# Performance work log

Measured on AMD Instinct MI355X. Metric: run time of the kernel, lower is better.

## Reference

```python
import jax, jax.numpy as jnp
import numpy as np

N = 50000      # nodes
E = 800000     # edges (avg degree 16)
DIN = 128
DH = 128
DOUT = 40
ALPHA = 0.1
BETA = 1.0


def gcn_conv(x, src, dst, ew, W, b, n):
    """PyG GCNConv: add self-loops, symmetric deg^-1/2 normalization, gather-scatter."""
    idx = jnp.arange(n)
    s = jnp.concatenate([src, idx])
    d = jnp.concatenate([dst, idx])
    w = jnp.concatenate([ew, jnp.ones((n,), x.dtype)])
    deg = jax.ops.segment_sum(w, d, num_segments=n)            # [N]
    dinv = jnp.where(deg > 0, jax.lax.rsqrt(deg), 0.0)
    norm = dinv[s] * w * dinv[d]                               # [E+N]
    h = x @ W                                                  # [N, dout]
    msg = h[s] * norm[:, None]                                 # gather + scale
    out = jax.ops.segment_sum(msg, d, num_segments=n)          # scatter-add
    return out + b


def setup_inputs() -> dict:
    key = jax.random.key(0)
    ks = jax.random.split(key, 10)
    x = jax.random.normal(ks[0], (N, DIN), jnp.float32)
    edge_index = jax.random.randint(ks[1], (2, E), 0, N, dtype=jnp.int64)
    edge_weight = jax.random.uniform(ks[2], (E,), jnp.float32)
    W1 = jax.random.normal(ks[3], (DIN, DH), jnp.float32) / np.float32(np.sqrt(DIN))
    b1 = jnp.zeros((DH,), jnp.float32)
    W2 = jax.random.normal(ks[4], (DH, DH), jnp.float32) / np.float32(np.sqrt(DH))
    b2 = jnp.zeros((DH,), jnp.float32)
    W3 = jax.random.normal(ks[5], (DH, DOUT), jnp.float32) / np.float32(np.sqrt(DH))
    b3 = jnp.zeros((DOUT,), jnp.float32)
    return {"x": x, "edge_index": edge_index, "edge_weight": edge_weight,
            "W1": W1, "b1": b1, "W2": W2, "b2": b2, "W3": W3, "b3": b3}


def reference(x, edge_index, edge_weight, W1, b1, W2, b2, W3, b3):
    src, dst = edge_index[0], edge_index[1]
    ones_w = jnp.ones((E,), x.dtype)
    h1 = jax.nn.relu(gcn_conv(x, src, dst, ones_w, W1, b1, N))   # conv1 (edge_weight=None)
    hc = gcn_conv(h1, src, dst, edge_weight, W2, b2, N)          # crf_layer with edge_weight
    h = ALPHA * h1 + BETA * hc                                   # weighted residual combo
    # LearnableBernoulliDropout: identity in eval mode
    out = gcn_conv(h, src, dst, ones_w, W3, b3, N)               # conv2
    return jax.nn.log_softmax(out, axis=1)
```

## Files before the change

kernel.cpp:

```cpp
#include <hip/hip_runtime.h>
#include <math.h>

#define DIN  128
#define DH   128
#define DOUT 40
#define ALPHA_C 0.1f
#define BETA_C  1.0f
#define SLOT 64

typedef __attribute__((ext_vector_type(8))) short short8;
typedef __attribute__((ext_vector_type(4))) float floatx4;

static inline int cdiv_h(int a, int b) { return (a + b - 1) / b; }

static __device__ __forceinline__ unsigned short f2b(float f) {
    unsigned u = __float_as_uint(f);
    u = u + 0x7FFFu + ((u >> 16) & 1u);
    return (unsigned short)(u >> 16);
}
static __device__ __forceinline__ unsigned pk2(float x, float y) {
    return (unsigned)f2b(x) | ((unsigned)f2b(y) << 16);
}
static __device__ __forceinline__ float2 b2f2(unsigned u) {
    float2 r;
    r.x = __uint_as_float(u << 16);
    r.y = __uint_as_float(u & 0xFFFF0000u);
    return r;
}
static __device__ __forceinline__ float b2f(unsigned short s) {
    return __uint_as_float(((unsigned)s) << 16);
}

__global__ __launch_bounds__(256) void build_slots(const int* __restrict__ src,
                                                   const int* __restrict__ dst,
                                                   const float* __restrict__ ew,
                                                   int* cnt,
                                                   int* __restrict__ csr_src,
                                                   float* __restrict__ csr_w, int E) {
    int e = blockIdx.x * 256 + threadIdx.x;
    if (e >= E) return;
    int d = dst[e];
    int pos = atomicAdd(&cnt[d], 1);
    if (pos < SLOT) {
        int base = (d << 6) + pos;
        csr_src[base] = src[e];
        csr_w[base] = ew[e];
    }
}

__global__ __launch_bounds__(256) void wdeg_dinv(const int* __restrict__ cnt,
                                                 const float* __restrict__ csr_w,
                                                 float* __restrict__ dinv1,
                                                 float* __restrict__ dinv2, int n) {
    int i = blockIdx.x * 256 + threadIdx.x;
    if (i >= n) return;
    int c = cnt[i]; if (c > SLOT) c = SLOT;
    dinv1[i] = rsqrtf((float)c + 1.f);
    float s = 1.f;
    int jb = i << 6;
    for (int j = 0; j < c; ++j) s += csr_w[jb + j];
    dinv2[i] = rsqrtf(s);
}

template <bool ABF16>
__global__ __launch_bounds__(256) void gemm128(const void* __restrict__ Ain,
                                               const float* __restrict__ W,
                                               unsigned short* __restrict__ C, int M) {
    __shared__ short As[128 * 128];
    __shared__ short Bs[128 * 128];
    int t = threadIdx.x;
    int blockM = blockIdx.x * 128;

    {
        int r = t >> 1, h = t & 1;
        int rg = blockM + r; if (rg > M - 1) rg = M - 1;
        if (ABF16) {
            const uint4* arow = (const uint4*)((const unsigned short*)Ain + (size_t)rg * 128);
            #pragma unroll
            for (int i = 0; i < 8; ++i) {
                int chunk = h * 8 + i;
                uint4 v = arow[chunk];
                *(uint4*)&As[r * 128 + ((chunk ^ (r & 7)) * 8)] = v;
            }
        } else {
            const float4* arow = (const float4*)((const float*)Ain + (size_t)rg * 128);
            #pragma unroll
            for (int i = 0; i < 8; ++i) {
                int chunk = h * 8 + i;
                float4 v0 = arow[chunk * 2], v1 = arow[chunk * 2 + 1];
                uint4 p;
                p.x = pk2(v0.x, v0.y); p.y = pk2(v0.z, v0.w);
                p.z = pk2(v1.x, v1.y); p.w = pk2(v1.z, v1.w);
                *(uint4*)&As[r * 128 + ((chunk ^ (r & 7)) * 8)] = p;
            }
        }
    }
    {
        int n = t & 127;
        int k0 = (t >> 7) * 64;
        #pragma unroll
        for (int it = 0; it < 8; ++it) {
            int k = k0 + it * 8;
            float f0 = W[(size_t)(k + 0) * 128 + n];
            float f1 = W[(size_t)(k + 1) * 128 + n];
            float f2 = W[(size_t)(k + 2) * 128 + n];
            float f3 = W[(size_t)(k + 3) * 128 + n];
            float f4 = W[(size_t)(k + 4) * 128 + n];
            float f5 = W[(size_t)(k + 5) * 128 + n];
            float f6 = W[(size_t)(k + 6) * 128 + n];
            float f7 = W[(size_t)(k + 7) * 128 + n];
            uint4 p;
            p.x = pk2(f0, f1); p.y = pk2(f2, f3);
            p.z = pk2(f4, f5); p.w = pk2(f6, f7);
            *(uint4*)&Bs[n * 128 + (((k >> 3) ^ (n & 7)) * 8)] = p;
        }
    }
    __syncthreads();

    int w = t >> 6, l = t & 63;
    int q = l >> 4, lm = l & 15;
    int rowoff = (w >> 1) * 64, coloff = (w & 1) * 64;

    floatx4 acc[4][4] = {};
    #pragma unroll
    for (int ks = 0; ks < 4; ++ks) {
        int chunk = ks * 4 + q;
        int sw = (chunk ^ (lm & 7)) * 8;
        short8 af[4], bf[4];
        #pragma unroll
        for (int tm = 0; tm < 4; ++tm)
            af[tm] = *(const short8*)&As[(rowoff + tm * 16 + lm) * 128 + sw];
        #pragma unroll
        for (int tn = 0; tn < 4; ++tn)
            bf[tn] = *(const short8*)&Bs[(coloff + tn * 16 + lm) * 128 + sw];
        #pragma unroll
        for (int tm = 0; tm < 4; ++tm)
            #pragma unroll
            for (int tn = 0; tn < 4; ++tn)
                acc[tm][tn] = __builtin_amdgcn_mfma_f32_16x16x32_bf16(af[tm], bf[tn], acc[tm][tn], 0, 0, 0);
    }

    #pragma unroll
    for (int tm = 0; tm < 4; ++tm) {
        #pragma unroll
        for (int reg = 0; reg < 4; ++reg) {
            int row = blockM + rowoff + tm * 16 + q * 4 + reg;
            if (row >= M) continue;
            #pragma unroll
            for (int tn = 0; tn < 4; ++tn) {
                int col = coloff + tn * 16 + lm;
                C[(size_t)row * 128 + col] = f2b(acc[tm][tn][reg]);
            }
        }
    }
}

__global__ __launch_bounds__(256) void gemm40(const unsigned short* __restrict__ Ain,
                                              const float* __restrict__ W,
                                              unsigned short* __restrict__ C, int M) {
    __shared__ short As[128 * 128];
    __shared__ short Bs[48 * 128];
    int t = threadIdx.x;
    int blockM = blockIdx.x * 128;

    {
        int r = t >> 1, h = t & 1;
        int rg = blockM + r; if (rg > M - 1) rg = M - 1;
        const uint4* arow = (const uint4*)(Ain + (size_t)rg * 128);
        #pragma unroll
        for (int i = 0; i < 8; ++i) {
            int chunk = h * 8 + i;
            uint4 v = arow[chunk];
            *(uint4*)&As[r * 128 + ((chunk ^ (r & 7)) * 8)] = v;
        }
    }
    {
        int n = t & 63;
        int k0 = (t >> 6) * 32;
        #pragma unroll
        for (int it = 0; it < 4; ++it) {
            int k = k0 + it * 8;
            uint4 p = {0, 0, 0, 0};
            if (n < 40) {
                float f0 = W[(size_t)(k + 0) * 40 + n];
                float f1 = W[(size_t)(k + 1) * 40 + n];
                float f2 = W[(size_t)(k + 2) * 40 + n];
                float f3 = W[(size_t)(k + 3) * 40 + n];
                float f4 = W[(size_t)(k + 4) * 40 + n];
                float f5 = W[(size_t)(k + 5) * 40 + n];
                float f6 = W[(size_t)(k + 6) * 40 + n];
                float f7 = W[(size_t)(k + 7) * 40 + n];
                p.x = pk2(f0, f1); p.y = pk2(f2, f3);
                p.z = pk2(f4, f5); p.w = pk2(f6, f7);
            }
            if (n < 48)
                *(uint4*)&Bs[n * 128 + (((k >> 3) ^ (n & 7)) * 8)] = p;
        }
    }
    __syncthreads();

    int w = t >> 6, l = t & 63;
    int q = l >> 4, lm = l & 15;
    int rowoff = w * 32;

    floatx4 acc[2][3] = {};
    #pragma unroll
    for (int ks = 0; ks < 4; ++ks) {
        int chunk = ks * 4 + q;
        int sw = (chunk ^ (lm & 7)) * 8;
        short8 af[2], bf[3];
        #pragma unroll
        for (int tm = 0; tm < 2; ++tm)
            af[tm] = *(const short8*)&As[(rowoff + tm * 16 + lm) * 128 + sw];
        #pragma unroll
        for (int tn = 0; tn < 3; ++tn)
            bf[tn] = *(const short8*)&Bs[(tn * 16 + lm) * 128 + sw];
        #pragma unroll
        for (int tm = 0; tm < 2; ++tm)
            #pragma unroll
            for (int tn = 0; tn < 3; ++tn)
                acc[tm][tn] = __builtin_amdgcn_mfma_f32_16x16x32_bf16(af[tm], bf[tn], acc[tm][tn], 0, 0, 0);
    }

    #pragma unroll
    for (int tm = 0; tm < 2; ++tm) {
        #pragma unroll
        for (int reg = 0; reg < 4; ++reg) {
            int row = blockM + rowoff + tm * 16 + q * 4 + reg;
            if (row >= M) continue;
            #pragma unroll
            for (int tn = 0; tn < 3; ++tn) {
                int col = tn * 16 + lm;
                if (col < 40) C[(size_t)row * 40 + col] = f2b(acc[tm][tn][reg]);
            }
        }
    }
}

template <int MODE>
__global__ __launch_bounds__(256) void agg128(const unsigned short* __restrict__ hpre,
                                              unsigned short* __restrict__ io,
                                              const float* __restrict__ bias,
                                              const float* __restrict__ dinv,
                                              const int* __restrict__ cnt,
                                              const int* __restrict__ csr_src,
                                              const float* __restrict__ csr_w, int n) {
    int row = blockIdx.x * 4 + (threadIdx.x >> 6);
    if (row >= n) return;
    int lane = threadIdx.x & 63;
    const unsigned* hp = (const unsigned*)hpre;

    float di = dinv[row];
    float d2 = di * di;
    float2 acc = b2f2(hp[(size_t)row * 64 + lane]);
    float2 bb = ((const float2*)bias)[lane];
    acc.x = fmaf(acc.x, d2, bb.x);
    acc.y = fmaf(acc.y, d2, bb.y);

    int c = cnt[row]; if (c > SLOT) c = SLOT;
    int jb = row << 6;
    int je = jb + c;

    int j = jb;
    for (; j + 3 < je; j += 4) {
        int s0 = csr_src[j], s1 = csr_src[j + 1], s2 = csr_src[j + 2], s3 = csr_src[j + 3];
        float c0, c1, c2, c3;
        if (MODE == 0) {
            c0 = dinv[s0] * di; c1 = dinv[s1] * di; c2 = dinv[s2] * di; c3 = dinv[s3] * di;
        } else {
            c0 = dinv[s0] * csr_w[j]     * di;
            c1 = dinv[s1] * csr_w[j + 1] * di;
            c2 = dinv[s2] * csr_w[j + 2] * di;
            c3 = dinv[s3] * csr_w[j + 3] * di;
        }
        float2 f0 = b2f2(hp[(size_t)s0 * 64 + lane]);
        float2 f1 = b2f2(hp[(size_t)s1 * 64 + lane]);
        float2 f2 = b2f2(hp[(size_t)s2 * 64 + lane]);
        float2 f3 = b2f2(hp[(size_t)s3 * 64 + lane]);
        acc.x = fmaf(c0, f0.x, acc.x); acc.y = fmaf(c0, f0.y, acc.y);
        acc.x = fmaf(c1, f1.x, acc.x); acc.y = fmaf(c1, f1.y, acc.y);
        acc.x = fmaf(c2, f2.x, acc.x); acc.y = fmaf(c2, f2.y, acc.y);
        acc.x = fmaf(c3, f3.x, acc.x); acc.y = fmaf(c3, f3.y, acc.y);
    }
    for (; j < je; ++j) {
        int s0 = csr_src[j];
        float c0 = (MODE == 0) ? dinv[s0] * di : dinv[s0] * csr_w[j] * di;
        float2 f0 = b2f2(hp[(size_t)s0 * 64 + lane]);
        acc.x = fmaf(c0, f0.x, acc.x); acc.y = fmaf(c0, f0.y, acc.y);
    }

    unsigned* iop = (unsigned*)io;
    if (MODE == 0) {
        acc.x = fmaxf(acc.x, 0.f); acc.y = fmaxf(acc.y, 0.f);
        iop[(size_t)row * 64 + lane] = pk2(acc.x, acc.y);
    } else {
        float2 h1 = b2f2(iop[(size_t)row * 64 + lane]);
        acc.x = fmaf(ALPHA_C, h1.x, BETA_C * acc.x);
        acc.y = fmaf(ALPHA_C, h1.y, BETA_C * acc.y);
        iop[(size_t)row * 64 + lane] = pk2(acc.x, acc.y);
    }
}

__global__ __launch_bounds__(256) void agg40_lsm(const unsigned short* __restrict__ hpre,
                                                 const float* __restrict__ bias,
                                                 const float* __restrict__ dinv,
                                                 const int* __restrict__ cnt,
                                                 const int* __restrict__ csr_src,
                                                 float* __restrict__ out, int n) {
    int row = blockIdx.x * 4 + (threadIdx.x >> 6);
    if (row >= n) return;
    int lane = threadIdx.x & 63;
    bool act = lane < DOUT;

    float di = dinv[row];
    float acc = 0.f;
    if (act) acc = b2f(hpre[(size_t)row * DOUT + lane]) * di * di + bias[lane];

    int c = cnt[row]; if (c > SLOT) c = SLOT;
    int jb = row << 6;
    int je = jb + c;

    int j = jb;
    for (; j + 3 < je; j += 4) {
        int s0 = csr_src[j], s1 = csr_src[j + 1], s2 = csr_src[j + 2], s3 = csr_src[j + 3];
        float c0 = dinv[s0] * di, c1 = dinv[s1] * di, c2 = dinv[s2] * di, c3 = dinv[s3] * di;
        float v0 = act ? b2f(hpre[(size_t)s0 * DOUT + lane]) : 0.f;
        float v1 = act ? b2f(hpre[(size_t)s1 * DOUT + lane]) : 0.f;
        float v2 = act ? b2f(hpre[(size_t)s2 * DOUT + lane]) : 0.f;
        float v3 = act ? b2f(hpre[(size_t)s3 * DOUT + lane]) : 0.f;
        acc = fmaf(c0, v0, acc);
        acc = fmaf(c1, v1, acc);
        acc = fmaf(c2, v2, acc);
        acc = fmaf(c3, v3, acc);
    }
    for (; j < je; ++j) {
        int s0 = csr_src[j];
        float c0 = dinv[s0] * di;
        float v0 = act ? b2f(hpre[(size_t)s0 * DOUT + lane]) : 0.f;
        acc = fmaf(c0, v0, acc);
    }

    float v = act ? acc : -INFINITY;
    float m = v;
    #pragma unroll
    for (int o = 32; o; o >>= 1) m = fmaxf(m, __shfl_xor(m, o, 64));
    float e = act ? expf(v - m) : 0.f;
    float s = e;
    #pragma unroll
    for (int o = 32; o; o >>= 1) s += __shfl_xor(s, o, 64);
    if (act) out[(size_t)row * DOUT + lane] = v - m - logf(s);
}

extern "C" void kernel_launch(void* const* d_in, const int* in_sizes, int n_in,
                              void* d_out, int out_size, void* d_ws, size_t ws_size,
                              hipStream_t stream) {
    const float* x   = (const float*)d_in[0];
    const int*   ei  = (const int*)  d_in[1];
    const float* ew  = (const float*)d_in[2];
    const float* W1  = (const float*)d_in[3];
    const float* b1  = (const float*)d_in[4];
    const float* W2  = (const float*)d_in[5];
    const float* b2  = (const float*)d_in[6];
    const float* W3  = (const float*)d_in[7];
    const float* b3  = (const float*)d_in[8];
    float* out = (float*)d_out;

    const int Nn = in_sizes[0] / DIN;
    const int E  = in_sizes[1] / 2;
    const int* src = ei;
    const int* dst = ei + E;

    char* wsb = (char*)d_ws;
    int*   cnt     = (int*)wsb;                          wsb += (size_t)Nn * 4;
    float* dinv1   = (float*)wsb;                        wsb += (size_t)Nn * 4;
    float* dinv2   = (float*)wsb;                        wsb += (size_t)Nn * 4;
    int*   csr_src = (int*)wsb;                          wsb += (size_t)Nn * SLOT * 4;
    float* csr_w   = (float*)wsb;                        wsb += (size_t)Nn * SLOT * 4;
    unsigned short* hpreb = (unsigned short*)wsb;        wsb += (size_t)Nn * DH * 2;
    unsigned short* h1b   = (unsigned short*)wsb;        wsb += (size_t)Nn * DH * 2;
    unsigned short* hp3b  = (unsigned short*)wsb;        wsb += (size_t)Nn * DOUT * 2;

    hipMemsetAsync(cnt, 0, (size_t)Nn * 4, stream);
    build_slots<<<cdiv_h(E, 256), 256, 0, stream>>>(src, dst, ew, cnt, csr_src, csr_w, E);
    wdeg_dinv<<<cdiv_h(Nn, 256), 256, 0, stream>>>(cnt, csr_w, dinv1, dinv2, Nn);

    int gemmGrid = cdiv_h(Nn, 128);
    int aggGrid = cdiv_h(Nn, 4);

    gemm128<false><<<gemmGrid, 256, 0, stream>>>(x, W1, hpreb, Nn);
    agg128<0><<<aggGrid, 256, 0, stream>>>(hpreb, h1b, b1, dinv1, cnt, csr_src, csr_w, Nn);

    gemm128<true><<<gemmGrid, 256, 0, stream>>>(h1b, W2, hpreb, Nn);
    agg128<1><<<aggGrid, 256, 0, stream>>>(hpreb, h1b, b2, dinv2, cnt, csr_src, csr_w, Nn);

    gemm40<<<gemmGrid, 256, 0, stream>>>(h1b, W3, hp3b, Nn);
    agg40_lsm<<<aggGrid, 256, 0, stream>>>(hp3b, b3, dinv1, cnt, csr_src, out, Nn);
}
```

Measured before the change: 312.9 us.

## Aggregate before the final projection and fuse log-softmax into the GEMM

The third GCN layer is reordered to aggregate the 128-wide features first (A·h) and then multiply by W3. This uses linearity and lets bias plus log-softmax be fused into the 40-column GEMM epilogue, which removes the separate agg40 kernel. The aggregation loop is also unrolled to 8 gathers so more loads are in flight. The cost is that the last gather now moves 128-wide rows instead of 40-wide ones, and the intermediate is rounded to bf16 at a different point.

New measurement: 290.1 us. 1.08x faster.

```diff
diff --git a/kernel.cpp b/kernel.cpp
--- a/kernel.cpp
+++ b/kernel.cpp
@@ -26,9 +26,6 @@
     r.x = __uint_as_float(u << 16);
     r.y = __uint_as_float(u & 0xFFFF0000u);
     return r;
-}
-static __device__ __forceinline__ float b2f(unsigned short s) {
-    return __uint_as_float(((unsigned)s) << 16);
 }
 
 __global__ __launch_bounds__(256) void build_slots(const int* __restrict__ src,
@@ -155,9 +152,10 @@
     }
 }
 
-__global__ __launch_bounds__(256) void gemm40(const unsigned short* __restrict__ Ain,
-                                              const float* __restrict__ W,
-                                              unsigned short* __restrict__ C, int M) {
+__global__ __launch_bounds__(256) void gemm40_lsm(const unsigned short* __restrict__ Ain,
+                                                  const float* __restrict__ W,
+                                                  const float* __restrict__ bias,
+                                                  float* __restrict__ out, int M) {
     __shared__ short As[128 * 128];
     __shared__ short Bs[48 * 128];
     int t = threadIdx.x;
@@ -222,16 +220,28 @@
                 acc[tm][tn] = __builtin_amdgcn_mfma_f32_16x16x32_bf16(af[tm], bf[tn], acc[tm][tn], 0, 0, 0);
     }
 
+    float bb0 = bias[lm];
+    float bb1 = bias[16 + lm];
+    float bb2 = (lm < 8) ? bias[32 + lm] : 0.f;
     #pragma unroll
     for (int tm = 0; tm < 2; ++tm) {
         #pragma unroll
         for (int reg = 0; reg < 4; ++reg) {
             int row = blockM + rowoff + tm * 16 + q * 4 + reg;
-            if (row >= M) continue;
-            #pragma unroll
-            for (int tn = 0; tn < 3; ++tn) {
-                int col = tn * 16 + lm;
-                if (col < 40) C[(size_t)row * 40 + col] = f2b(acc[tm][tn][reg]);
+            float v0 = acc[tm][0][reg] + bb0;
+            float v1 = acc[tm][1][reg] + bb1;
+            float v2 = (lm < 8) ? acc[tm][2][reg] + bb2 : -INFINITY;
+            float mx = fmaxf(fmaxf(v0, v1), v2);
+            #pragma unroll
+            for (int o = 1; o < 16; o <<= 1) mx = fmaxf(mx, __shfl_xor(mx, o, 64));
+            float ss = expf(v0 - mx) + expf(v1 - mx) + ((lm < 8) ? expf(v2 - mx) : 0.f);
+            #pragma unroll
+            for (int o = 1; o < 16; o <<= 1) ss += __shfl_xor(ss, o, 64);
+            float ls = mx + logf(ss);
+            if (row < M) {
+                out[(size_t)row * 40 + lm]      = v0 - ls;
+                out[(size_t)row * 40 + 16 + lm] = v1 - ls;
+                if (lm < 8) out[(size_t)row * 40 + 32 + lm] = v2 - ls;
             }
         }
     }
@@ -253,102 +263,67 @@
     float di = dinv[row];
     float d2 = di * di;
     float2 acc = b2f2(hp[(size_t)row * 64 + lane]);
-    float2 bb = ((const float2*)bias)[lane];
-    acc.x = fmaf(acc.x, d2, bb.x);
-    acc.y = fmaf(acc.y, d2, bb.y);
+    if (MODE == 2) {
+        acc.x *= d2; acc.y *= d2;
+    } else {
+        float2 bb = ((const float2*)bias)[lane];
+        acc.x = fmaf(acc.x, d2, bb.x);
+        acc.y = fmaf(acc.y, d2, bb.y);
+    }
 
     int c = cnt[row]; if (c > SLOT) c = SLOT;
     int jb = row << 6;
     int je = jb + c;
-
     int j = jb;
-    for (; j + 3 < je; j += 4) {
-        int s0 = csr_src[j], s1 = csr_src[j + 1], s2 = csr_src[j + 2], s3 = csr_src[j + 3];
-        float c0, c1, c2, c3;
-        if (MODE == 0) {
-            c0 = dinv[s0] * di; c1 = dinv[s1] * di; c2 = dinv[s2] * di; c3 = dinv[s3] * di;
-        } else {
-            c0 = dinv[s0] * csr_w[j]     * di;
-            c1 = dinv[s1] * csr_w[j + 1] * di;
-            c2 = dinv[s2] * csr_w[j + 2] * di;
-            c3 = dinv[s3] * csr_w[j + 3] * di;
-        }
-        float2 f0 = b2f2(hp[(size_t)s0 * 64 + lane]);
-        float2 f1 = b2f2(hp[(size_t)s1 * 64 + lane]);
-        float2 f2 = b2f2(hp[(size_t)s2 * 64 + lane]);
-        float2 f3 = b2f2(hp[(size_t)s3 * 64 + lane]);
-        acc.x = fmaf(c0, f0.x, acc.x); acc.y = fmaf(c0, f0.y, acc.y);
-        acc.x = fmaf(c1, f1.x, acc.x); acc.y = fmaf(c1, f1.y, acc.y);
-        acc.x = fmaf(c2, f2.x, acc.x); acc.y = fmaf(c2, f2.y, acc.y);
-        acc.x = fmaf(c3, f3.x, acc.x); acc.y = fmaf(c3, f3.y, acc.y);
+
+    while (j + 8 <= je) {
+        int ss[8]; float2 ff[8];
+        #pragma unroll
+        for (int u = 0; u < 8; ++u) ss[u] = csr_src[j + u];
+        #pragma unroll
+        for (int u = 0; u < 8; ++u) ff[u] = b2f2(hp[(size_t)ss[u] * 64 + lane]);
+        #pragma unroll
+        for (int u = 0; u < 8; ++u) {
+            float cc = (MODE == 1) ? dinv[ss[u]] * csr_w[j + u] * di : dinv[ss[u]] * di;
+            acc.x = fmaf(cc, ff[u].x, acc.x);
+            acc.y = fmaf(cc, ff[u].y, acc.y);
+        }
+        j += 8;
+    }
+    if (j + 4 <= je) {
+        int ss[4]; float2 ff[4];
+        #pragma unroll
+        for (int u = 0; u < 4; ++u) ss[u] = csr_src[j + u];
+        #pragma unroll
+        for (int u = 0; u < 4; ++u) ff[u] = b2f2(hp[(size_t)ss[u] * 64 + lane]);
+        #pragma unroll
+        for (int u = 0; u < 4; ++u) {
+            float cc = (MODE == 1) ? dinv[ss[u]] * csr_w[j + u] * di : dinv[ss[u]] * di;
+            acc.x = fmaf(cc, ff[u].x, acc.x);
+            acc.y = fmaf(cc, ff[u].y, acc.y);
+        }
+        j += 4;
     }
     for (; j < je; ++j) {
         int s0 = csr_src[j];
-        float c0 = (MODE == 0) ? dinv[s0] * di : dinv[s0] * csr_w[j] * di;
+        float cc = (MODE == 1) ? dinv[s0] * csr_w[j] * di : dinv[s0] * di;
         float2 f0 = b2f2(hp[(size_t)s0 * 64 + lane]);
-        acc.x = fmaf(c0, f0.x, acc.x); acc.y = fmaf(c0, f0.y, acc.y);
+        acc.x = fmaf(cc, f0.x, acc.x);
+        acc.y = fmaf(cc, f0.y, acc.y);
     }
 
     unsigned* iop = (unsigned*)io;
     if (MODE == 0) {
         acc.x = fmaxf(acc.x, 0.f); acc.y = fmaxf(acc.y, 0.f);
         iop[(size_t)row * 64 + lane] = pk2(acc.x, acc.y);
-    } else {
+    } else if (MODE == 1) {
         float2 h1 = b2f2(iop[(size_t)row * 64 + lane]);
         acc.x = fmaf(ALPHA_C, h1.x, BETA_C * acc.x);
         acc.y = fmaf(ALPHA_C, h1.y, BETA_C * acc.y);
         iop[(size_t)row * 64 + lane] = pk2(acc.x, acc.y);
-    }
-}
-
-__global__ __launch_bounds__(256) void agg40_lsm(const unsigned short* __restrict__ hpre,
-                                                 const float* __restrict__ bias,
-                                                 const float* __restrict__ dinv,
-                                                 const int* __restrict__ cnt,
-                                                 const int* __restrict__ csr_src,
-                                                 float* __restrict__ out, int n) {
-    int row = blockIdx.x * 4 + (threadIdx.x >> 6);
-    if (row >= n) return;
-    int lane = threadIdx.x & 63;
-    bool act = lane < DOUT;
-
-    float di = dinv[row];
-    float acc = 0.f;
-    if (act) acc = b2f(hpre[(size_t)row * DOUT + lane]) * di * di + bias[lane];
-
-    int c = cnt[row]; if (c > SLOT) c = SLOT;
-    int jb = row << 6;
-    int je = jb + c;
-
-    int j = jb;
-    for (; j + 3 < je; j += 4) {
-        int s0 = csr_src[j], s1 = csr_src[j + 1], s2 = csr_src[j + 2], s3 = csr_src[j + 3];
-        float c0 = dinv[s0] * di, c1 = dinv[s1] * di, c2 = dinv[s2] * di, c3 = dinv[s3] * di;
-        float v0 = act ? b2f(hpre[(size_t)s0 * DOUT + lane]) : 0.f;
-        float v1 = act ? b2f(hpre[(size_t)s1 * DOUT + lane]) : 0.f;
-        float v2 = act ? b2f(hpre[(size_t)s2 * DOUT + lane]) : 0.f;
-        float v3 = act ? b2f(hpre[(size_t)s3 * DOUT + lane]) : 0.f;
-        acc = fmaf(c0, v0, acc);
-        acc = fmaf(c1, v1, acc);
-        acc = fmaf(c2, v2, acc);
-        acc = fmaf(c3, v3, acc);
-    }
-    for (; j < je; ++j) {
-        int s0 = csr_src[j];
-        float c0 = dinv[s0] * di;
-        float v0 = act ? b2f(hpre[(size_t)s0 * DOUT + lane]) : 0.f;
-        acc = fmaf(c0, v0, acc);
-    }
-
-    float v = act ? acc : -INFINITY;
-    float m = v;
-    #pragma unroll
-    for (int o = 32; o; o >>= 1) m = fmaxf(m, __shfl_xor(m, o, 64));
-    float e = act ? expf(v - m) : 0.f;
-    float s = e;
-    #pragma unroll
-    for (int o = 32; o; o >>= 1) s += __shfl_xor(s, o, 64);
-    if (act) out[(size_t)row * DOUT + lane] = v - m - logf(s);
+    } else {
+        iop[(size_t)row * 64 + lane] = pk2(acc.x, acc.y);
+    }
 }
 
 extern "C" void kernel_launch(void* const* d_in, const int* in_sizes, int n_in,
@@ -378,7 +353,6 @@
     float* csr_w   = (float*)wsb;                        wsb += (size_t)Nn * SLOT * 4;
     unsigned short* hpreb = (unsigned short*)wsb;        wsb += (size_t)Nn * DH * 2;
     unsigned short* h1b   = (unsigned short*)wsb;        wsb += (size_t)Nn * DH * 2;
-    unsigned short* hp3b  = (unsigned short*)wsb;        wsb += (size_t)Nn * DOUT * 2;
 
     hipMemsetAsync(cnt, 0, (size_t)Nn * 4, stream);
     build_slots<<<cdiv_h(E, 256), 256, 0, stream>>>(src, dst, ew, cnt, csr_src, csr_w, E);
@@ -393,6 +367,6 @@
     gemm128<true><<<gemmGrid, 256, 0, stream>>>(h1b, W2, hpreb, Nn);
     agg128<1><<<aggGrid, 256, 0, stream>>>(hpreb, h1b, b2, dinv2, cnt, csr_src, csr_w, Nn);
 
-    gemm40<<<gemmGrid, 256, 0, stream>>>(h1b, W3, hp3b, Nn);
-    agg40_lsm<<<aggGrid, 256, 0, stream>>>(hp3b, b3, dinv1, cnt, csr_src, out, Nn);
-}
+    agg128<2><<<aggGrid, 256, 0, stream>>>(h1b, hpreb, b3, dinv1, cnt, csr_src, csr_w, Nn);
+    gemm40_lsm<<<gemmGrid, 256, 0, stream>>>(hpreb, W3, b3, out, Nn);
+}
```
